# Kernel optimization log

Hardware: AMD Instinct MI355X
Metric: run time of the kernel (lower is better)

## Reference

```python
import jax, jax.numpy as jnp
import numpy as np

NH, NOPE_D, ROPE_D, V_D, R = 16, 48, 16, 64, 128
EPS = 1e-6

def rms_norm(x, w):
    norm = jax.lax.rsqrt(jnp.mean(jnp.square(x), axis=-1, keepdims=True) + EPS)
    return x * norm * w

def apply_rope(x, cos, sin):
    # x: (..., rope_d); cos/sin broadcastable (..., rope_d//2)
    d = x.shape[-1]
    x1, x2 = x[..., : d // 2], x[..., d // 2 :]
    return jnp.concatenate([x1 * cos - x2 * sin, x2 * cos + x1 * sin], axis=-1)

def setup_inputs() -> dict:
    key = jax.random.key(0)
    ks = jax.random.split(key, 8)
    B, T, D = 2, 2048, 1024
    s = lambda fan_in: 1.0 / np.sqrt(fan_in)
    return {
        "x": jax.random.normal(ks[0], (B, T, D), jnp.float32),
        "cos": jax.random.uniform(ks[1], (T, ROPE_D // 2), jnp.float32),
        "sin": jax.random.uniform(ks[2], (T, ROPE_D // 2), jnp.float32),
        "Wq": jax.random.normal(ks[3], (NH * (NOPE_D + ROPE_D), D), jnp.float32) * s(D),
        "q_norm_w": jnp.ones((NOPE_D + ROPE_D,), jnp.float32),
        "Wkva": jax.random.normal(ks[4], (R + ROPE_D, D), jnp.float32) * s(D),
        "kva_norm_w": jnp.ones((R,), jnp.float32),
        "Wkvb": jax.random.normal(ks[5], (NH * (NOPE_D + V_D), R), jnp.float32) * s(R),
        "Wo": jax.random.normal(ks[6], (D, NH * V_D), jnp.float32) * s(NH * V_D),
    }

def reference(x, cos, sin, Wq, q_norm_w, Wkva, kva_norm_w, Wkvb, Wo):
    B, T, D = x.shape
    # Q path: project, per-head RMSNorm over (nope+rope) dims, split
    q = (x @ Wq.T).reshape(B, T, NH, NOPE_D + ROPE_D)
    q = rms_norm(q, q_norm_w)
    q_nope, q_rope = q[..., :NOPE_D], q[..., NOPE_D:]
    # Low-rank KV path
    kv_a = x @ Wkva.T  # (B,T,R+ROPE_D)
    kv_latent = rms_norm(kv_a[..., :R], kva_norm_w)
    k_rope_raw = kv_a[..., R:]  # (B,T,ROPE_D) shared across heads
    kv_b = (kv_latent @ Wkvb.T).reshape(B, T, NH, NOPE_D + V_D)
    k_nope, v = kv_b[..., :NOPE_D], kv_b[..., NOPE_D:]
    # Decoupled RoPE
    cos_t = cos[None, :T, None, :]  # (1,T,1,rope_d/2)
    sin_t = sin[None, :T, None, :]
    q_rope = apply_rope(q_rope, cos_t, sin_t)
    k_rope = apply_rope(k_rope_raw[:, :, None, :], cos[None, :T, None, :], sin[None, :T, None, :])
    k_rope = jnp.broadcast_to(k_rope, (B, T, NH, ROPE_D))
    q_full = jnp.concatenate([q_nope, q_rope], axis=-1)  # (B,T,NH,64)
    k_full = jnp.concatenate([k_nope, k_rope], axis=-1)
    # Causal attention, scale = 1/sqrt(nope+rope)
    scale = (NOPE_D + ROPE_D) ** -0.5
    scores = jnp.einsum("bqhd,bkhd->bhqk", q_full, k_full) * scale
    causal = jnp.tril(jnp.ones((T, T), bool))
    scores = jnp.where(causal[None, None], scores, -jnp.inf)
    attn = jax.nn.softmax(scores, axis=-1)
    out = jnp.einsum("bhqk,bkhd->bqhd", attn, v).reshape(B, T, NH * V_D)
    return out @ Wo.T
```

## Files before the change

### kernel.cpp

```cpp
#include <hip/hip_runtime.h>
#include <hip/hip_bf16.h>
#include <math.h>

#define NH 16
#define T_ 2048
#define B_ 2
#define D_ 1024
#define EPS 1e-6f

typedef __attribute__((ext_vector_type(8))) short bf16x8;
typedef __attribute__((ext_vector_type(4))) float f32x4;

__device__ __forceinline__ float wred_sum(float v){
  #pragma unroll
  for (int o = 32; o > 0; o >>= 1) v += __shfl_xor(v, o, 64);
  return v;
}

__device__ __forceinline__ unsigned pack_bf16(float a, float b){
  __hip_bfloat162 t = __float22bfloat162_rn(make_float2(a, b));
  unsigned r; __builtin_memcpy(&r, &t, 4); return r;
}

__device__ __forceinline__ void gload_lds16(const void* g, void* l){
  __builtin_amdgcn_global_load_lds((const __attribute__((address_space(1))) void*)g,
                                   (__attribute__((address_space(3))) void*)l, 16, 0, 0);
}

__global__ __launch_bounds__(256)
void cvt5(const float* __restrict__ x, const float* __restrict__ wq,
          const float* __restrict__ wkva, const float* __restrict__ wkvb,
          const float* __restrict__ wo,
          __hip_bfloat16* __restrict__ xb, __hip_bfloat16* __restrict__ wqb,
          __hip_bfloat16* __restrict__ wkvab, __hip_bfloat16* __restrict__ wkvbb,
          __hip_bfloat16* __restrict__ wob)
{
  const int i = blockIdx.x * 256 + threadIdx.x;
  const float* s; __hip_bfloat16* d; size_t soff, doff;
  if      (i < 1048576) { s = x;    d = xb;    soff = doff = i; }
  else if (i < 1310720) { s = wq;   d = wqb;   soff = doff = i - 1048576; }
  else if (i < 1347584) { s = wkva; d = wkvab; soff = doff = i - 1310720; }
  else if (i < 1404928) {
    const int off = i - 1347584;
    const int srow = off >> 5, c4 = off & 31;
    const int h = srow / 112, dd = srow % 112;
    const int drow = (dd < 48) ? (h*48 + dd) : (768 + h*64 + (dd - 48));
    s = wkvb; d = wkvbb; soff = off; doff = (size_t)drow*32 + c4;
  }
  else                  { s = wo;   d = wob;   soff = doff = i - 1404928; }
  float4 v = *(const float4*)(s + soff * 4);
  *(__hip_bfloat162*)(d + doff * 4)     = __float22bfloat162_rn(make_float2(v.x, v.y));
  *(__hip_bfloat162*)(d + doff * 4 + 2) = __float22bfloat162_rn(make_float2(v.z, v.w));
}

template<typename CT>
__global__ __launch_bounds__(256, 2)
void gemm_bt64(const __hip_bfloat16* __restrict__ A, const __hip_bfloat16* __restrict__ W,
               CT* __restrict__ C, int M, int N, int K)
{
  __shared__ __hip_bfloat16 As[2][128 * 64];
  __shared__ __hip_bfloat16 Ws[2][64 * 64];
  const int tid = threadIdx.x;
  const int wv = tid >> 6, lane = tid & 63;
  const int m = lane & 15, quad = lane >> 4;
  const int bm = blockIdx.y * 128, bn = blockIdx.x * 64;

  const __hip_bfloat16* ga[4];
  const __hip_bfloat16* gw[2];
  #pragma unroll
  for (int i = 0; i < 4; i++) {
    const int slot = i*256 + tid;
    const int row = slot >> 3, cb = slot & 7;
    ga[i] = A + (size_t)(bm + row) * K + ((cb ^ (row & 7)) << 3);
  }
  #pragma unroll
  for (int i = 0; i < 2; i++) {
    const int slot = i*256 + tid;
    const int row = slot >> 3, cb = slot & 7;
    int wr = bn + row; if (wr >= N) wr = N - 1;
    gw[i] = W + (size_t)wr * K + ((cb ^ (row & 7)) << 3);
  }
  auto stage = [&](int buf){
    #pragma unroll
    for (int i = 0; i < 4; i++) { gload_lds16(ga[i], &As[buf][(i*256 + wv*64)*8]); ga[i] += 64; }
    #pragma unroll
    for (int i = 0; i < 2; i++) { gload_lds16(gw[i], &Ws[buf][(i*256 + wv*64)*8]); gw[i] += 64; }
  };

  f32x4 acc[2][4];
  #pragma unroll
  for (int mi = 0; mi < 2; mi++)
    #pragma unroll
    for (int nj = 0; nj < 4; nj++) acc[mi][nj] = (f32x4){0.f,0.f,0.f,0.f};

  stage(0);
  const int iters = K >> 6;
  for (int it = 0; it < iters; it++) {
    const int cur = it & 1;
    __syncthreads();
    if (it + 1 < iters) stage(cur ^ 1);
    #pragma unroll
    for (int ks = 0; ks < 2; ks++) {
      const int cb = ((ks*4 + quad) ^ (m & 7)) << 3;
      bf16x8 af[2], wf[4];
      #pragma unroll
      for (int mi = 0; mi < 2; mi++)
        af[mi] = *(const bf16x8*)(&As[cur][(wv*32 + mi*16 + m) * 64 + cb]);
      #pragma unroll
      for (int nj = 0; nj < 4; nj++)
        wf[nj] = *(const bf16x8*)(&Ws[cur][(nj*16 + m) * 64 + cb]);
      #pragma unroll
      for (int mi = 0; mi < 2; mi++)
        #pragma unroll
        for (int nj = 0; nj < 4; nj++)
          acc[mi][nj] = __builtin_amdgcn_mfma_f32_16x16x32_bf16(af[mi], wf[nj], acc[mi][nj], 0, 0, 0);
    }
  }

  #pragma unroll
  for (int mi = 0; mi < 2; mi++)
    #pragma unroll
    for (int nj = 0; nj < 4; nj++) {
      const int col = bn + nj*16 + m;
      if (col < N) {
        #pragma unroll
        for (int r = 0; r < 4; r++) {
          const int row = bm + wv*32 + mi*16 + quad*4 + r;
          if constexpr (sizeof(CT) == 2)
            C[(size_t)row * N + col] = (CT)__float2bfloat16(acc[mi][nj][r]);
          else
            C[(size_t)row * N + col] = acc[mi][nj][r];
        }
      }
    }
}

__global__ __launch_bounds__(256, 2)
void gemm_qkva(const __hip_bfloat16* __restrict__ A, const __hip_bfloat16* __restrict__ Wqb,
               const __hip_bfloat16* __restrict__ Wkvab,
               const float* __restrict__ qw, const float* __restrict__ cosp,
               const float* __restrict__ sinp,
               __hip_bfloat16* __restrict__ qb, float* __restrict__ kva)
{
  __shared__ __hip_bfloat16 As[2][128 * 64];
  __shared__ __hip_bfloat16 Ws[2][64 * 64];
  const int K = 1024;
  const int tid = threadIdx.x;
  const int wv = tid >> 6, lane = tid & 63;
  const int m = lane & 15, quad = lane >> 4;
  const int bm = blockIdx.y * 128;
  const bool isq = blockIdx.x < 16;
  const __hip_bfloat16* W = isq ? Wqb : Wkvab;
  const int bn = isq ? blockIdx.x*64 : (blockIdx.x - 16)*64;
  const int Nw = isq ? 1024 : 144;

  const __hip_bfloat16* ga[4];
  const __hip_bfloat16* gw[2];
  #pragma unroll
  for (int i = 0; i < 4; i++) {
    const int slot = i*256 + tid;
    const int row = slot >> 3, cb = slot & 7;
    ga[i] = A + (size_t)(bm + row) * K + ((cb ^ (row & 7)) << 3);
  }
  #pragma unroll
  for (int i = 0; i < 2; i++) {
    const int slot = i*256 + tid;
    const int row = slot >> 3, cb = slot & 7;
    int wr = bn + row; if (wr >= Nw) wr = Nw - 1;
    gw[i] = W + (size_t)wr * K + ((cb ^ (row & 7)) << 3);
  }
  auto stage = [&](int buf){
    #pragma unroll
    for (int i = 0; i < 4; i++) { gload_lds16(ga[i], &As[buf][(i*256 + wv*64)*8]); ga[i] += 64; }
    #pragma unroll
    for (int i = 0; i < 2; i++) { gload_lds16(gw[i], &Ws[buf][(i*256 + wv*64)*8]); gw[i] += 64; }
  };

  f32x4 acc[2][4];
  #pragma unroll
  for (int mi = 0; mi < 2; mi++)
    #pragma unroll
    for (int nj = 0; nj < 4; nj++) acc[mi][nj] = (f32x4){0.f,0.f,0.f,0.f};

  stage(0);
  for (int it = 0; it < 16; it++) {
    const int cur = it & 1;
    __syncthreads();
    if (it < 15) stage(cur ^ 1);
    #pragma unroll
    for (int ks = 0; ks < 2; ks++) {
      const int cb = ((ks*4 + quad) ^ (m & 7)) << 3;
      bf16x8 af[2], wf[4];
      #pragma unroll
      for (int mi = 0; mi < 2; mi++)
        af[mi] = *(const bf16x8*)(&As[cur][(wv*32 + mi*16 + m) * 64 + cb]);
      #pragma unroll
      for (int nj = 0; nj < 4; nj++)
        wf[nj] = *(const bf16x8*)(&Ws[cur][(nj*16 + m) * 64 + cb]);
      #pragma unroll
      for (int mi = 0; mi < 2; mi++)
        #pragma unroll
        for (int nj = 0; nj < 4; nj++)
          acc[mi][nj] = __builtin_amdgcn_mfma_f32_16x16x32_bf16(af[mi], wf[nj], acc[mi][nj], 0, 0, 0);
    }
  }

  if (isq) {
    const int head = blockIdx.x;
    float qwv[4];
    #pragma unroll
    for (int nj = 0; nj < 4; nj++) qwv[nj] = qw[nj*16 + m];
    const int j = m & 7;
    const float qscale = 0.125f * 1.44269504f;
    #pragma unroll
    for (int mi = 0; mi < 2; mi++) {
      #pragma unroll
      for (int r = 0; r < 4; r++) {
        float ss = 0.f;
        #pragma unroll
        for (int nj = 0; nj < 4; nj++) { const float t = acc[mi][nj][r]; ss = fmaf(t, t, ss); }
        ss += __shfl_xor(ss, 1, 64); ss += __shfl_xor(ss, 2, 64);
        ss += __shfl_xor(ss, 4, 64); ss += __shfl_xor(ss, 8, 64);
        const float nrm = rsqrtf(ss * (1.0f/64.0f) + EPS);
        float v[4];
        #pragma unroll
        for (int nj = 0; nj < 4; nj++) v[nj] = acc[mi][nj][r] * nrm * qwv[nj];
        const int grow = bm + wv*32 + mi*16 + quad*4 + r;
        const int t = grow & (T_ - 1);
        const int b = grow >> 11;
        const float part = __shfl_xor(v[3], 8, 64);
        const float c = cosp[t*8 + j], sn = sinp[t*8 + j];
        v[3] = (m < 8) ? (v[3]*c - part*sn) : (v[3]*c + part*sn);
        __hip_bfloat16* dst = qb + ((size_t)(b*NH + head)*T_ + t)*64 + m;
        #pragma unroll
        for (int nj = 0; nj < 4; nj++) dst[nj*16] = __float2bfloat16(v[nj] * qscale);
      }
    }
  } else {
    #pragma unroll
    for (int mi = 0; mi < 2; mi++)
      #pragma unroll
      for (int nj = 0; nj < 4; nj++) {
        const int col = bn + nj*16 + m;
        if (col < 144) {
          #pragma unroll
          for (int r = 0; r < 4; r++) {
            const int row = bm + wv*32 + mi*16 + quad*4 + r;
            kva[(size_t)row * 144 + col] = acc[mi][nj][r];
          }
        }
      }
  }
}

__global__ void prep_kv(const float* __restrict__ kva, const float* __restrict__ kw,
                        const float* __restrict__ cosp, const float* __restrict__ sinp,
                        __hip_bfloat16* __restrict__ kvl16, __hip_bfloat16* __restrict__ krope16)
{
  const int tid = threadIdx.x;
  const int bt = blockIdx.x;
  const int t = bt % T_;
  const float* row = kva + (size_t)bt * 144;
  const float v = row[tid];
  float s = wred_sum(v * v);
  __shared__ float red[2];
  if ((tid & 63) == 0) red[tid >> 6] = s;
  __syncthreads();
  const float total = red[0] + red[1];
  const float norm = rsqrtf(total * (1.0f/128.0f) + EPS);
  kvl16[(size_t)bt * 128 + tid] = __float2bfloat16(v * norm * kw[tid]);
  if (tid < 16) {
    const int j = tid & 7;
    const float c = cosp[t*8 + j], sn = sinp[t*8 + j];
    const float x1 = row[128 + j], x2 = row[136 + j];
    krope16[(size_t)bt * 16 + tid] = __float2bfloat16((tid < 8) ? (x1 * c - x2 * sn)
                                                               : (x2 * c + x1 * sn));
  }
}

__global__ __launch_bounds__(256, 2)
void gemm_kvb(const __hip_bfloat16* __restrict__ A, const __hip_bfloat16* __restrict__ W,
              __hip_bfloat16* __restrict__ knope, __hip_bfloat16* __restrict__ vt)
{
  __shared__ __hip_bfloat16 As[2][128 * 64];
  __shared__ __hip_bfloat16 Ws[2][64 * 64];
  const int K = 128;
  const int tid = threadIdx.x;
  const int wv = tid >> 6, lane = tid & 63;
  const int m = lane & 15, quad = lane >> 4;
  const int bm = blockIdx.y * 128, bn = blockIdx.x * 64;

  const __hip_bfloat16* ga[4];
  const __hip_bfloat16* gw[2];
  #pragma unroll
  for (int i = 0; i < 4; i++) {
    const int slot = i*256 + tid;
    const int row = slot >> 3, cb = slot & 7;
    ga[i] = A + (size_t)(bm + row) * K + ((cb ^ (row & 7)) << 3);
  }
  #pragma unroll
  for (int i = 0; i < 2; i++) {
    const int slot = i*256 + tid;
    const int row = slot >> 3, cb = slot & 7;
    gw[i] = W + (size_t)(bn + row) * K + ((cb ^ (row & 7)) << 3);
  }
  auto stage = [&](int buf){
    #pragma unroll
    for (int i = 0; i < 4; i++) { gload_lds16(ga[i], &As[buf][(i*256 + wv*64)*8]); ga[i] += 64; }
    #pragma unroll
    for (int i = 0; i < 2; i++) { gload_lds16(gw[i], &Ws[buf][(i*256 + wv*64)*8]); gw[i] += 64; }
  };

  f32x4 acc[2][4];
  #pragma unroll
  for (int mi = 0; mi < 2; mi++)
    #pragma unroll
    for (int nj = 0; nj < 4; nj++) acc[mi][nj] = (f32x4){0.f,0.f,0.f,0.f};

  stage(0);
  for (int it = 0; it < 2; it++) {
    const int cur = it & 1;
    __syncthreads();
    if (it == 0) stage(1);
    #pragma unroll
    for (int ks = 0; ks < 2; ks++) {
      const int cb = ((ks*4 + quad) ^ (m & 7)) << 3;
      bf16x8 af[2], wf[4];
      #pragma unroll
      for (int mi = 0; mi < 2; mi++)
        af[mi] = *(const bf16x8*)(&As[cur][(wv*32 + mi*16 + m) * 64 + cb]);
      #pragma unroll
      for (int nj = 0; nj < 4; nj++)
        wf[nj] = *(const bf16x8*)(&Ws[cur][(nj*16 + m) * 64 + cb]);
      #pragma unroll
      for (int mi = 0; mi < 2; mi++)
        #pragma unroll
        for (int nj = 0; nj < 4; nj++)
          acc[mi][nj] = __builtin_amdgcn_mfma_f32_16x16x32_bf16(af[mi], wf[nj], acc[mi][nj], 0, 0, 0);
    }
  }

  if (bn < 768) {
    #pragma unroll
    for (int mi = 0; mi < 2; mi++)
      #pragma unroll
      for (int nj = 0; nj < 4; nj++) {
        const int col = bn + nj*16 + m;
        #pragma unroll
        for (int r = 0; r < 4; r++) {
          const int row = bm + wv*32 + mi*16 + quad*4 + r;
          knope[(size_t)row * 768 + col] = __float2bfloat16(acc[mi][nj][r]);
        }
      }
  } else {
    __syncthreads();
    short* TL = (short*)&As[0][0];
    #pragma unroll
    for (int mi = 0; mi < 2; mi++)
      #pragma unroll
      for (int nj = 0; nj < 4; nj++) {
        const int d = nj*16 + m;
        #pragma unroll
        for (int r = 0; r < 4; r++) {
          const int tl = wv*32 + mi*16 + quad*4 + r;
          __hip_bfloat16 hv = __float2bfloat16(acc[mi][nj][r]);
          short sv; __builtin_memcpy(&sv, &hv, 2);
          TL[d*136 + tl] = sv;
        }
      }
    __syncthreads();
    const int h = (bn - 768) >> 6;
    const int b = bm >> 11;
    const int t0 = bm & (T_ - 1);
    #pragma unroll
    for (int i = 0; i < 4; i++) {
      const int unit = i*256 + tid;
      const int d = unit >> 4, tu = unit & 15;
      *(bf16x8*)(vt + ((size_t)(b*NH + h)*64 + d)*T_ + t0 + tu*8)
          = *(const bf16x8*)(TL + d*136 + tu*8);
    }
  }
}

__device__ __forceinline__ void fa_store(float lrun, f32x4 (&oacc)[4],
    const int b, const int qrow0, const int h, const int m, const int quad,
    __hip_bfloat16* __restrict__ aout)
{
  lrun += __shfl_xor(lrun, 16, 64);
  lrun += __shfl_xor(lrun, 32, 64);
  float lr[4];
  #pragma unroll
  for (int r = 0; r < 4; r++) lr[r] = __shfl(lrun, (quad << 2) | r, 64);
  #pragma unroll
  for (int vs = 0; vs < 4; vs++)
    #pragma unroll
    for (int r = 0; r < 4; r++)
      aout[(size_t)(b*T_ + qrow0 + quad*4 + r) * 1024 + h*64 + vs*16 + m]
          = __float2bfloat16(oacc[vs][r] / lr[r]);
}

__global__ __launch_bounds__(256, 4)
void attn_tile(const __hip_bfloat16* __restrict__ qb,
               const __hip_bfloat16* __restrict__ knope,
               const __hip_bfloat16* __restrict__ krope16,
               const __hip_bfloat16* __restrict__ vt16,
               __hip_bfloat16* __restrict__ aout)
{
  __shared__ __hip_bfloat16 SL[16384];
  const int tid = threadIdx.x;
  const int wv = tid >> 6, lane = tid & 63;
  const int m = lane & 15, quad = lane >> 4;
  const int idx = (blockIdx.x + blockIdx.y) & 31;
  const int pj = idx & 7, pk = idx >> 3;
  const int qt = (pk == 0) ? pj : (pk == 1) ? (15 - pj) : (pk == 2) ? (16 + pj) : (31 - pj);
  const int bh = blockIdx.y;
  const int b = bh >> 4, h = bh & 15;
  const int qbase = qt*64 + wv*16;
  const int nt = qt + 1;

  const __hip_bfloat16* qr = qb + ((size_t)bh*T_ + qbase + m)*64 + quad*8;
  const bf16x8 q0 = *(const bf16x8*)qr, q1 = *(const bf16x8*)(qr + 32);

  const __hip_bfloat16* pK[2]; size_t iK[2];
  const __hip_bfloat16* pV[2];
  #pragma unroll
  for (int i = 0; i < 2; i++) {
    const int slot = i*256 + tid;
    const int krow = slot >> 3;
    const int kde = (slot & 7) ^ (krow & 7);
    if (kde < 6) { pK[i] = knope + (size_t)(b*T_ + krow)*768 + h*48 + kde*8; iK[i] = (size_t)64*768; }
    else         { pK[i] = krope16 + (size_t)(b*T_ + krow)*16 + (kde-6)*8;   iK[i] = (size_t)64*16; }
    pV[i] = vt16 + ((size_t)bh*64 + krow)*T_ + kde*8;
  }

  auto stage = [&](int buf){
    #pragma unroll
    for (int i = 0; i < 2; i++) {
      gload_lds16(pK[i], SL + buf*4096 + (i*256 + wv*64)*8);
      gload_lds16(pV[i], SL + 8192 + buf*4096 + (i*256 + wv*64)*8);
      pK[i] += iK[i]; pV[i] += 64;
    }
  };

  f32x4 o[4];
  #pragma unroll
  for (int vs = 0; vs < 4; vs++) o[vs] = (f32x4){0.f,0.f,0.f,0.f};
  float lrun = 0.f;

  const int sw0 = quad ^ (m & 7);
  stage(0);

  for (int kt = 0; kt < nt; kt++) {
    const int cur = kt & 1;
    __syncthreads();
    const __hip_bfloat16* Kc = SL + cur*4096;
    const __hip_bfloat16* Vc = SL + 8192 + cur*4096;
    const bool dtile = (kt == qt);

    f32x4 s[4];
    #pragma unroll
    for (int sub = 0; sub < 4; sub++) {
      if (!dtile || sub <= wv) {
        const bf16x8 kf0 = *(const bf16x8*)(Kc + (sub*16 + m)*64 + sw0*8);
        const bf16x8 kf1 = *(const bf16x8*)(Kc + (sub*16 + m)*64 + (sw0^4)*8);
        f32x4 z = (f32x4){0.f,0.f,0.f,0.f};
        z = __builtin_amdgcn_mfma_f32_16x16x32_bf16(kf0, q0, z, 0, 0, 0);
        z = __builtin_amdgcn_mfma_f32_16x16x32_bf16(kf1, q1, z, 0, 0, 0);
        s[sub] = z;
      } else {
        s[sub] = (f32x4){-1e30f,-1e30f,-1e30f,-1e30f};
      }
    }

    if (kt + 1 < nt) stage(cur ^ 1);

    if (dtile) {
      #pragma unroll
      for (int sub = 0; sub < 4; sub++) {
        if (sub == wv) {
          #pragma unroll
          for (int r = 0; r < 4; r++)
            if (quad*4 + r > m) s[sub][r] = -1e30f;
        }
      }
    }

    float p[4][4];
    #pragma unroll
    for (int sub = 0; sub < 4; sub++)
      #pragma unroll
      for (int r = 0; r < 4; r++) {
        const float e = exp2f(s[sub][r] - 48.0f);
        p[sub][r] = e; lrun += e;
      }

    unsigned u[4][2];
    #pragma unroll
    for (int sub = 0; sub < 4; sub++) {
      u[sub][0] = pack_bf16(p[sub][0], p[sub][1]);
      u[sub][1] = pack_bf16(p[sub][2], p[sub][3]);
    }
    bf16x8 a[2];
    #pragma unroll
    for (int c = 0; c < 2; c++) {
      union { int i[4]; bf16x8 v; } au;
      #pragma unroll
      for (int w4 = 0; w4 < 4; w4++) {
        const int src = (((2*quad + (w4 >> 1)) & 3) << 4) | m;
        const int lo = __shfl((int)u[c*2][w4 & 1], src, 64);
        const int hi = __shfl((int)u[c*2+1][w4 & 1], src, 64);
        au.i[w4] = (quad & 2) ? hi : lo;
      }
      a[c] = au.v;
    }

    #pragma unroll
    for (int vs = 0; vs < 4; vs++)
      #pragma unroll
      for (int c = 0; c < 2; c++) {
        const bf16x8 vf = *(const bf16x8*)(Vc + (vs*16 + m)*64 + (((c*4 + quad) ^ (m & 7)) << 3));
        o[vs] = __builtin_amdgcn_mfma_f32_16x16x32_bf16(a[c], vf, o[vs], 0, 0, 0);
      }
  }

  fa_store(lrun, o, b, qbase, h, m, quad, aout);
}

extern "C" void kernel_launch(void* const* d_in, const int* in_sizes, int n_in,
                              void* d_out, int out_size, void* d_ws, size_t ws_size,
                              hipStream_t stream)
{
  const float* x    = (const float*)d_in[0];
  const float* cosp = (const float*)d_in[1];
  const float* sinp = (const float*)d_in[2];
  const float* Wq   = (const float*)d_in[3];
  const float* qw   = (const float*)d_in[4];
  const float* Wkva = (const float*)d_in[5];
  const float* kw   = (const float*)d_in[6];
  const float* Wkvb = (const float*)d_in[7];
  const float* Wo   = (const float*)d_in[8];
  float* out = (float*)d_out;

  float* kva = (float*)d_ws;
  __hip_bfloat16* xb16    = (__hip_bfloat16*)(kva + 589824);
  __hip_bfloat16* knope16 = xb16 + 4194304;
  __hip_bfloat16* kvl16   = knope16 + 3145728;
  __hip_bfloat16* qb16    = kvl16 + 524288;
  __hip_bfloat16* vt16    = qb16 + 4194304;
  __hip_bfloat16* krope16 = vt16 + 4194304;
  __hip_bfloat16* Wqb     = krope16 + 65536;
  __hip_bfloat16* Wkvab   = Wqb + 1048576;
  __hip_bfloat16* Wkvbb   = Wkvab + 147456;
  __hip_bfloat16* Wob     = Wkvbb + 229376;
  __hip_bfloat16* ab16    = Wob + 1048576;

  const int M = B_ * T_;

  cvt5<<<6512, 256, 0, stream>>>(x, Wq, Wkva, Wkvb, Wo, xb16, Wqb, Wkvab, Wkvbb, Wob);
  gemm_qkva<<<dim3(19, 32), 256, 0, stream>>>(xb16, Wqb, Wkvab, qw, cosp, sinp, qb16, kva);
  prep_kv<<<M, 128, 0, stream>>>(kva, kw, cosp, sinp, kvl16, krope16);
  gemm_kvb<<<dim3(28, 32), 256, 0, stream>>>(kvl16, Wkvbb, knope16, vt16);
  attn_tile<<<dim3(32, B_ * NH), 256, 0, stream>>>(qb16, knope16, krope16, vt16, ab16);
  gemm_bt64<float><<<dim3(16, 32), 256, 0, stream>>>(ab16, Wob, out, M, 1024, 1024);
}
```

Measured before the change: 183.8 us.

## Compute PV as transposed 16x16x16 MFMA to drop P shuffles

Result: faster. 178.7 us (-2.8%).

```diff
diff --git a/kernel.cpp b/kernel.cpp
--- a/kernel.cpp
+++ b/kernel.cpp
@@ -9,6 +9,7 @@
 #define EPS 1e-6f
 
 typedef __attribute__((ext_vector_type(8))) short bf16x8;
+typedef __attribute__((ext_vector_type(4))) short bf16x4;
 typedef __attribute__((ext_vector_type(4))) float f32x4;
 
 __device__ __forceinline__ float wred_sum(float v){
@@ -25,6 +26,15 @@
 __device__ __forceinline__ void gload_lds16(const void* g, void* l){
   __builtin_amdgcn_global_load_lds((const __attribute__((address_space(1))) void*)g,
                                    (__attribute__((address_space(3))) void*)l, 16, 0, 0);
+}
+
+__device__ __forceinline__ f32x4 mfma16(bf16x4 a, bf16x4 b, f32x4 c){
+#if __has_builtin(__builtin_amdgcn_mfma_f32_16x16x16bf16_1k)
+  return __builtin_amdgcn_mfma_f32_16x16x16bf16_1k(a, b, c, 0, 0, 0);
+#else
+  asm volatile("v_mfma_f32_16x16x16_bf16 %0, %1, %2, %0" : "+v"(c) : "v"(a), "v"(b));
+  return c;
+#endif
 }
 
 __global__ __launch_bounds__(256)
@@ -382,21 +392,21 @@
   }
 }
 
-__device__ __forceinline__ void fa_store(float lrun, f32x4 (&oacc)[4],
-    const int b, const int qrow0, const int h, const int m, const int quad,
+__device__ __forceinline__ void fa_store_t(float lrun, f32x4 (&o)[4],
+    const int b, const int qbase, const int h, const int m, const int quad,
     __hip_bfloat16* __restrict__ aout)
 {
   lrun += __shfl_xor(lrun, 16, 64);
   lrun += __shfl_xor(lrun, 32, 64);
-  float lr[4];
-  #pragma unroll
-  for (int r = 0; r < 4; r++) lr[r] = __shfl(lrun, (quad << 2) | r, 64);
-  #pragma unroll
-  for (int vs = 0; vs < 4; vs++)
-    #pragma unroll
-    for (int r = 0; r < 4; r++)
-      aout[(size_t)(b*T_ + qrow0 + quad*4 + r) * 1024 + h*64 + vs*16 + m]
-          = __float2bfloat16(oacc[vs][r] / lr[r]);
+  const float inv = 1.0f / lrun;
+  const size_t base = (size_t)(b*T_ + qbase + m) * 1024 + h*64 + quad*4;
+  #pragma unroll
+  for (int vs = 0; vs < 4; vs++) {
+    union { unsigned ui[2]; bf16x4 v; } pk;
+    pk.ui[0] = pack_bf16(o[vs][0] * inv, o[vs][1] * inv);
+    pk.ui[1] = pack_bf16(o[vs][2] * inv, o[vs][3] * inv);
+    *(bf16x4*)(aout + base + vs*16) = pk.v;
+  }
 }
 
 __global__ __launch_bounds__(256, 4)
@@ -448,16 +458,19 @@
   float lrun = 0.f;
 
   const int sw0 = quad ^ (m & 7);
+  const int qh = quad >> 1, ql = quad & 1;
   stage(0);
 
   for (int kt = 0; kt < nt; kt++) {
     const int cur = kt & 1;
     __syncthreads();
+    if (kt + 1 < nt) stage(cur ^ 1);
     const __hip_bfloat16* Kc = SL + cur*4096;
     const __hip_bfloat16* Vc = SL + 8192 + cur*4096;
     const bool dtile = (kt == qt);
 
     f32x4 s[4];
+    __builtin_amdgcn_s_setprio(1);
     #pragma unroll
     for (int sub = 0; sub < 4; sub++) {
       if (!dtile || sub <= wv) {
@@ -471,8 +484,7 @@
         s[sub] = (f32x4){-1e30f,-1e30f,-1e30f,-1e30f};
       }
     }
-
-    if (kt + 1 < nt) stage(cur ^ 1);
+    __builtin_amdgcn_s_setprio(0);
 
     if (dtile) {
       #pragma unroll
@@ -485,45 +497,34 @@
       }
     }
 
-    float p[4][4];
-    #pragma unroll
-    for (int sub = 0; sub < 4; sub++)
-      #pragma unroll
-      for (int r = 0; r < 4; r++) {
-        const float e = exp2f(s[sub][r] - 48.0f);
-        p[sub][r] = e; lrun += e;
-      }
-
-    unsigned u[4][2];
+    bf16x4 u[4];
     #pragma unroll
     for (int sub = 0; sub < 4; sub++) {
-      u[sub][0] = pack_bf16(p[sub][0], p[sub][1]);
-      u[sub][1] = pack_bf16(p[sub][2], p[sub][3]);
-    }
-    bf16x8 a[2];
-    #pragma unroll
-    for (int c = 0; c < 2; c++) {
-      union { int i[4]; bf16x8 v; } au;
-      #pragma unroll
-      for (int w4 = 0; w4 < 4; w4++) {
-        const int src = (((2*quad + (w4 >> 1)) & 3) << 4) | m;
-        const int lo = __shfl((int)u[c*2][w4 & 1], src, 64);
-        const int hi = __shfl((int)u[c*2+1][w4 & 1], src, 64);
-        au.i[w4] = (quad & 2) ? hi : lo;
-      }
-      a[c] = au.v;
-    }
-
-    #pragma unroll
-    for (int vs = 0; vs < 4; vs++)
-      #pragma unroll
-      for (int c = 0; c < 2; c++) {
-        const bf16x8 vf = *(const bf16x8*)(Vc + (vs*16 + m)*64 + (((c*4 + quad) ^ (m & 7)) << 3));
-        o[vs] = __builtin_amdgcn_mfma_f32_16x16x32_bf16(a[c], vf, o[vs], 0, 0, 0);
-      }
-  }
-
-  fa_store(lrun, o, b, qbase, h, m, quad, aout);
+      float p0 = exp2f(s[sub][0] - 48.0f), p1 = exp2f(s[sub][1] - 48.0f);
+      float p2 = exp2f(s[sub][2] - 48.0f), p3 = exp2f(s[sub][3] - 48.0f);
+      lrun += (p0 + p1) + (p2 + p3);
+      union { unsigned ui[2]; bf16x4 v; } uu;
+      uu.ui[0] = pack_bf16(p0, p1);
+      uu.ui[1] = pack_bf16(p2, p3);
+      u[sub] = uu.v;
+    }
+
+    __builtin_amdgcn_s_setprio(1);
+    #pragma unroll
+    for (int vs = 0; vs < 4; vs++) {
+      #pragma unroll
+      for (int sub = 0; sub < 4; sub++) {
+        if (!dtile || sub <= wv) {
+          const bf16x4 vf = *(const bf16x4*)(Vc + (vs*16 + m)*64
+                              + (((sub*2 + qh) ^ (m & 7)) << 3) + (ql << 2));
+          o[vs] = mfma16(vf, u[sub], o[vs]);
+        }
+      }
+    }
+    __builtin_amdgcn_s_setprio(0);
+  }
+
+  fa_store_t(lrun, o, b, qbase, h, m, quad, aout);
 }
 
 extern "C" void kernel_launch(void* const* d_in, const int* in_sizes, int n_in,
```
